# Kernel tuning notes

Measured on AMD Instinct MI355X. Metric: run time of the kernel, lower is better.

Reference implementation:

```python
import jax, jax.numpy as jnp
import numpy as np

B, T, C, H, N = 4, 1024, 1024, 16, 64
DW, DA, DV, DG = 64, 64, 64, 160  # LoRA ranks derived from C=1024
LNX_EPS = 0.00064


def layer_norm(h, g, b, eps=1e-5):
    m = h.mean(-1, keepdims=True)
    var = ((h - m) ** 2).mean(-1, keepdims=True)
    return (h - m) * jax.lax.rsqrt(var + eps) * g + b


def token_shift(h):
    # nn.ZeroPad2d((0,0,1,-1)): shift right along T, zero at t=0
    return jnp.pad(h, ((0, 0), (1, 0), (0, 0)))[:, :-1]


def wkv7(r, w, k, v, a, b):
    # RWKV-7 generalized recurrence. Inputs [B,T,C]; w is log-space decay.
    def re(t):
        return t.reshape(B, T, H, N).transpose(1, 0, 2, 3)  # -> [T,B,H,N]
    r, w, k, v, a, b = map(re, (r, w, k, v, a, b))
    dec = jnp.exp(-jnp.exp(w))
    S0 = jnp.zeros((B, H, N, N), r.dtype)  # state: [value_dim, key_dim]
    def step(S, ins):
        r_, d_, k_, v_, a_, b_ = ins
        sa = jnp.einsum('bhij,bhj->bhi', S, a_)
        S = S * d_[:, :, None, :] + sa[..., None] * b_[:, :, None, :] + v_[..., None] * k_[:, :, None, :]
        return S, jnp.einsum('bhij,bhj->bhi', S, r_)
    _, out = jax.lax.scan(step, S0, (r, dec, k, v, a, b))
    return out.transpose(1, 0, 2, 3).reshape(B, T, C)


def _forward(x, v_first, ln1_g, ln1_b, ln2_g, ln2_b, x_r, x_w, x_k_mix, x_v_mix, x_a, x_g,
             w0, w1, w2, a0, a1, a2, v0, v1, v2, g1, g2, k_k, k_a, r_k,
             W_r, W_k, W_v, W_o, lnx_g, lnx_b, xk_c, Wk_ff, Wv_ff):
    # ---- RNW_Tmix (original RWKV-7 path, layer_id > 0) ----
    h = layer_norm(x, ln1_g, ln1_b)
    xx = token_shift(h) - h
    xr = h + xx * x_r
    xw = h + xx * x_w
    xk = h + xx * x_k_mix
    xv = h + xx * x_v_mix
    xa = h + xx * x_a
    xg = h + xx * x_g
    r = xr @ W_r.T
    w = -jax.nn.softplus(-(w0 + jnp.tanh(xw @ w1) @ w2)) - 0.5
    k = xk @ W_k.T
    v = xv @ W_v.T
    v = v + (v_first - v) * jax.nn.sigmoid(v0 + (xv @ v1) @ v2)
    a = jax.nn.sigmoid(a0 + (xa @ a1) @ a2)
    g = jax.nn.sigmoid(xg @ g1) @ g2
    kk = (k * k_k).reshape(B, T, H, N)
    kk = kk / jnp.maximum(jnp.linalg.norm(kk, axis=-1, keepdims=True), 1e-12)
    kk = kk.reshape(B, T, C)
    k = k * (1 + (a - 1) * k_a)
    y = wkv7(r, w, k, v, -kk, kk * a)
    # GroupNorm(H groups of N channels), eps=0.00064
    yg = y.reshape(B, T, H, N)
    m = yg.mean(-1, keepdims=True)
    var = ((yg - m) ** 2).mean(-1, keepdims=True)
    y = ((yg - m) * jax.lax.rsqrt(var + LNX_EPS)).reshape(B, T, C) * lnx_g + lnx_b
    r4 = r.reshape(B, T, H, N)
    k4 = k.reshape(B, T, H, N)
    v4 = v.reshape(B, T, H, N)
    y = y + ((r4 * k4 * r_k).sum(-1, keepdims=True) * v4).reshape(B, T, C)
    x = x + (y * g) @ W_o.T
    # ---- RWKV_CMix_x070 ----
    h2 = layer_norm(x, ln2_g, ln2_b)
    hx = token_shift(h2) - h2
    kf = h2 + hx * xk_c
    kf = jnp.square(jax.nn.relu(kf @ Wk_ff.T))
    x = x + kf @ Wv_ff.T
    return x


def setup_inputs() -> dict:
    key = jax.random.key(0)
    ks = jax.random.split(key, 40)
    it = iter(range(40))
    def rn(shape, s=0.02):
        return (jax.random.normal(ks[next(it)], shape) * s).astype(jnp.float32)
    def ru(shape):
        return jax.random.uniform(ks[next(it)], shape).astype(jnp.float32)
    return {
        'x': rn((B, T, C), 1.0),
        'v_first': rn((B, T, C), 1.0),
        'ln1_g': jnp.ones((C,), jnp.float32), 'ln1_b': jnp.zeros((C,), jnp.float32),
        'ln2_g': jnp.ones((C,), jnp.float32), 'ln2_b': jnp.zeros((C,), jnp.float32),
        'x_r': ru((1, 1, C)), 'x_w': ru((1, 1, C)), 'x_k_mix': ru((1, 1, C)),
        'x_v_mix': ru((1, 1, C)), 'x_a': ru((1, 1, C)), 'x_g': ru((1, 1, C)),
        'w0': rn((1, 1, C), 0.5) - 4.0, 'w1': rn((C, DW)), 'w2': rn((DW, C), 0.1),
        'a0': rn((1, 1, C), 0.3), 'a1': rn((C, DA)), 'a2': rn((DA, C), 0.1),
        'v0': rn((1, 1, C), 0.3) + 0.73, 'v1': rn((C, DV)), 'v2': rn((DV, C), 0.1),
        'g1': rn((C, DG)), 'g2': rn((DG, C), 0.1),
        'k_k': rn((1, 1, C), 0.05) + 0.71, 'k_a': rn((1, 1, C), 0.05) + 1.02,
        'r_k': rn((H, N), 0.05) - 0.04,
        'W_r': rn((C, C)), 'W_k': rn((C, C), 0.002), 'W_v': rn((C, C)), 'W_o': rn((C, C)),
        'lnx_g': jnp.ones((C,), jnp.float32), 'lnx_b': jnp.zeros((C,), jnp.float32),
        'xk_c': ru((1, 1, C)),
        'Wk_ff': rn((4 * C, C)), 'Wv_ff': rn((C, 4 * C)),
    }


def reference(x, v_first, ln1_g, ln1_b, ln2_g, ln2_b, x_r, x_w, x_k_mix, x_v_mix, x_a, x_g,
              w0, w1, w2, a0, a1, a2, v0, v1, v2, g1, g2, k_k, k_a, r_k,
              W_r, W_k, W_v, W_o, lnx_g, lnx_b, xk_c, Wk_ff, Wv_ff):
    return _forward(x, v_first, ln1_g, ln1_b, ln2_g, ln2_b, x_r, x_w, x_k_mix, x_v_mix, x_a, x_g,
                    w0, w1, w2, a0, a1, a2, v0, v1, v2, g1, g2, k_k, k_a, r_k,
                    W_r, W_k, W_v, W_o, lnx_g, lnx_b, xk_c, Wk_ff, Wv_ff)
```

## Files before the change

kernel.cpp:

```cpp
#include <hip/hip_runtime.h>
#include <hip/hip_bf16.h>


#define BB 4
#define TT 1024
#define CC 1024
#define HH 16
#define NHEAD 64
#define MTOK 4096
#define FFDIM 4096

using bf16 = __hip_bfloat16;
typedef __attribute__((ext_vector_type(8))) short short8;
typedef __attribute__((ext_vector_type(4))) float f32x4;

__device__ __forceinline__ float b2f(bf16 x) { return __bfloat162float(x); }
__device__ __forceinline__ bf16 f2b(float x) { return __float2bfloat16(x); }
__device__ __forceinline__ float u2f(unsigned short u) {
  return __uint_as_float((unsigned)u << 16);
}
__device__ __forceinline__ float4 cv4(ushort4 u) {
  return make_float4(u2f(u.x), u2f(u.y), u2f(u.z), u2f(u.w));
}
__device__ __forceinline__ float ldin(const void* p, size_t i, int m) {
  return m ? b2f(((const bf16*)p)[i]) : ((const float*)p)[i];
}

__device__ __forceinline__ void async16(const void* g, void* l) {
  __builtin_amdgcn_global_load_lds((const __attribute__((address_space(1))) void*)g,
                                   (__attribute__((address_space(3))) void*)l, 16, 0, 0);
}

__device__ __forceinline__ float rowsum16(float x) {
  int t;
  t = __builtin_amdgcn_update_dpp(0, __float_as_int(x), 0x121, 0xF, 0xF, true);
  x += __int_as_float(t);
  t = __builtin_amdgcn_update_dpp(0, __float_as_int(x), 0x122, 0xF, 0xF, true);
  x += __int_as_float(t);
  t = __builtin_amdgcn_update_dpp(0, __float_as_int(x), 0x124, 0xF, 0xF, true);
  x += __int_as_float(t);
  t = __builtin_amdgcn_update_dpp(0, __float_as_int(x), 0x128, 0xF, 0xF, true);
  x += __int_as_float(t);
  return x;
}

__device__ __forceinline__ void rowsum16_2(float& x, float& y) {
  int t1, t2;
  t1 = __builtin_amdgcn_update_dpp(0, __float_as_int(x), 0x121, 0xF, 0xF, true);
  t2 = __builtin_amdgcn_update_dpp(0, __float_as_int(y), 0x121, 0xF, 0xF, true);
  x += __int_as_float(t1); y += __int_as_float(t2);
  t1 = __builtin_amdgcn_update_dpp(0, __float_as_int(x), 0x122, 0xF, 0xF, true);
  t2 = __builtin_amdgcn_update_dpp(0, __float_as_int(y), 0x122, 0xF, 0xF, true);
  x += __int_as_float(t1); y += __int_as_float(t2);
  t1 = __builtin_amdgcn_update_dpp(0, __float_as_int(x), 0x124, 0xF, 0xF, true);
  t2 = __builtin_amdgcn_update_dpp(0, __float_as_int(y), 0x124, 0xF, 0xF, true);
  x += __int_as_float(t1); y += __int_as_float(t2);
  t1 = __builtin_amdgcn_update_dpp(0, __float_as_int(x), 0x128, 0xF, 0xF, true);
  t2 = __builtin_amdgcn_update_dpp(0, __float_as_int(y), 0x128, 0xF, 0xF, true);
  x += __int_as_float(t1); y += __int_as_float(t2);
}

__global__ void probe_kernel(const unsigned int* g, int* flag) {
  if (threadIdx.x == 0 && blockIdx.x == 0) {
    flag[0] = (g[0] == 0x3F800000u) ? 0 : 1;
    flag[1] = 1;
  }
}

__global__ __launch_bounds__(256) void cvt_all(
    const void* wr, const void* wk, const void* wv, const void* wo,
    const void* wkff, const void* wvff, const int* flagp,
    bf16* wrc, bf16* wkc, bf16* wvc, bf16* woc, bf16* wkffc, bf16* wvffc) {
  const int z = blockIdx.z;
  const void* in; bf16* out; int n4;
  const int nCC4 = CC * CC / 4, nFF4 = FFDIM * CC / 4;
  switch (z) {
    case 0: in = wr;   out = wrc;   n4 = nCC4; break;
    case 1: in = wk;   out = wkc;   n4 = nCC4; break;
    case 2: in = wv;   out = wvc;   n4 = nCC4; break;
    case 3: in = wo;   out = woc;   n4 = nCC4; break;
    case 4: in = wkff; out = wkffc; n4 = nFF4; break;
    default: in = wvff; out = wvffc; n4 = nFF4; break;
  }
  const int fl = *flagp;
  const int i4 = blockIdx.x * 256 + threadIdx.x;
  if (i4 >= n4) return;
  const size_t i = (size_t)i4 * 4;
#pragma unroll
  for (int e = 0; e < 4; ++e) out[i + e] = f2b(ldin(in, i + e, fl));
}

__global__ __launch_bounds__(256) void fillmark_kernel(unsigned short* out, int n) {
  const int i = blockIdx.x * 256 + threadIdx.x;
  if (i < n) out[i] = 0x3F80;
}

template<int XM>
__global__ __launch_bounds__(256) void ln_kernel(const void* __restrict__ x,
    const void* __restrict__ g, const void* __restrict__ be, const int* flagp,
    bf16* __restrict__ out, float eps) {
  const int fl = *flagp;
  const int xm = (XM < 0) ? fl : XM;
  const int tid = threadIdx.x;
  const size_t base = (size_t)blockIdx.x * CC + tid * 4;
  float v[4];
#pragma unroll
  for (int e = 0; e < 4; ++e) v[e] = ldin(x, base + e, xm);
  float s  = v[0] + v[1] + v[2] + v[3];
  float ss = v[0]*v[0] + v[1]*v[1] + v[2]*v[2] + v[3]*v[3];
#pragma unroll
  for (int m = 1; m <= 32; m <<= 1) { s += __shfl_xor(s, m); ss += __shfl_xor(ss, m); }
  __shared__ float red[8];
  const int wave = tid >> 6, lane = tid & 63;
  if (lane == 0) { red[wave] = s; red[4 + wave] = ss; }
  __syncthreads();
  s  = red[0] + red[1] + red[2] + red[3];
  ss = red[4] + red[5] + red[6] + red[7];
  const float mean = s * (1.0f / CC);
  const float var  = ss * (1.0f / CC) - mean * mean;
  const float rstd = rsqrtf(var + eps);
#pragma unroll
  for (int e = 0; e < 4; ++e) {
    const int c = tid * 4 + e;
    out[base + e] = f2b((v[e] - mean) * rstd * ldin(g, c, fl) + ldin(be, c, fl));
  }
}

__global__ __launch_bounds__(256) void mix6_kernel(const bf16* __restrict__ h,
    const void* cr, const void* cw, const void* ck,
    const void* cv, const void* ca, const void* cg, const int* flagp,
    bf16* __restrict__ xr, bf16* __restrict__ xw, bf16* __restrict__ xk,
    bf16* __restrict__ xv, bf16* __restrict__ xa, bf16* __restrict__ xg) {
  const int fl = *flagp;
  const size_t idx = (size_t)blockIdx.x * 256 + threadIdx.x;
  const int c = idx & (CC - 1);
  const int t = (idx >> 10) & (TT - 1);
  const float hv = b2f(h[idx]);
  const float xx = (t == 0 ? 0.f : b2f(h[idx - CC])) - hv;
  xr[idx] = f2b(hv + xx * ldin(cr, c, fl));
  xw[idx] = f2b(hv + xx * ldin(cw, c, fl));
  xk[idx] = f2b(hv + xx * ldin(ck, c, fl));
  xv[idx] = f2b(hv + xx * ldin(cv, c, fl));
  xa[idx] = f2b(hv + xx * ldin(ca, c, fl));
  xg[idx] = f2b(hv + xx * ldin(cg, c, fl));
}

__global__ __launch_bounds__(256) void mix1_kernel(const bf16* __restrict__ h,
    const void* cf, const int* flagp, bf16* __restrict__ out) {
  const int fl = *flagp;
  const size_t idx = (size_t)blockIdx.x * 256 + threadIdx.x;
  const int c = idx & (CC - 1);
  const int t = (idx >> 10) & (TT - 1);
  const float hv = b2f(h[idx]);
  const float xx = (t == 0 ? 0.f : b2f(h[idx - CC])) - hv;
  out[idx] = f2b(hv + xx * ldin(cf, c, fl));
}

__global__ __launch_bounds__(256) void transpose_all(
    const void* w1, const void* a1, const void* v1, const void* g1,
    const void* w2, const void* a2, const void* v2, const void* g2,
    const int* flagp,
    bf16* w1t, bf16* a1t, bf16* v1t, bf16* g1t,
    bf16* w2t, bf16* a2t, bf16* v2t, bf16* g2t) {
  const int z = blockIdx.z;
  const void* in; bf16* out; int R, Cc;
  switch (z) {
    case 0: in = w1; out = w1t; R = CC;  Cc = 64;  break;
    case 1: in = a1; out = a1t; R = CC;  Cc = 64;  break;
    case 2: in = v1; out = v1t; R = CC;  Cc = 64;  break;
    case 3: in = g1; out = g1t; R = CC;  Cc = 160; break;
    case 4: in = w2; out = w2t; R = 64;  Cc = CC;  break;
    case 5: in = a2; out = a2t; R = 64;  Cc = CC;  break;
    case 6: in = v2; out = v2t; R = 64;  Cc = CC;  break;
    default: in = g2; out = g2t; R = 160; Cc = CC; break;
  }
  const int fl = *flagp;
  const int idx = blockIdx.x * 256 + threadIdx.x;
  if (idx >= R * Cc) return;
  const int r = idx / Cc, c = idx - r * Cc;
  out[(size_t)c * R + r] = f2b(ldin(in, idx, fl));
}

__device__ __forceinline__ void gemm_core(const bf16* __restrict__ A,
    const bf16* __restrict__ Bm, bf16* __restrict__ Out, int M, int N, int K,
    int mode, short* As, short* Bs) {
  const int tid  = threadIdx.x;
  const int wave = tid >> 6;
  const int lane = tid & 63;
  const int m0 = blockIdx.y * 128;
  const int n0 = blockIdx.x * 128;
  const int wr = (wave >> 1) * 64;
  const int wc = (wave & 1) * 64;
  const int lrow = lane & 15;
  const int lq   = lane >> 4;
  f32x4 acc[4][4];
#pragma unroll
  for (int i = 0; i < 4; ++i)
#pragma unroll
    for (int j = 0; j < 4; ++j) acc[i][j] = (f32x4){0.f, 0.f, 0.f, 0.f};

  for (int k0 = 0; k0 < K; k0 += 32) {
#pragma unroll
    for (int j = 0; j < 2; ++j) {
      const int chunk = j * 256 + tid;
      const int row = chunk >> 2;
      const int c8  = (chunk & 3) * 8;
      const int ldsbase = (j * 256 + wave * 64) * 8;
      const bf16* ga = A + (size_t)(m0 + row) * K + (k0 + c8);
      int br = n0 + row; br = br < N ? br : N - 1;
      const bf16* gb = Bm + (size_t)br * K + (k0 + c8);
      async16(ga, &As[ldsbase]);
      async16(gb, &Bs[ldsbase]);
    }
    __syncthreads();
    short8 af[4], bfr[4];
#pragma unroll
    for (int mi = 0; mi < 4; ++mi)
      af[mi] = *(const short8*)&As[(wr + mi * 16 + lrow) * 32 + lq * 8];
#pragma unroll
    for (int ni = 0; ni < 4; ++ni)
      bfr[ni] = *(const short8*)&Bs[(wc + ni * 16 + lrow) * 32 + lq * 8];
#pragma unroll
    for (int mi = 0; mi < 4; ++mi)
#pragma unroll
      for (int ni = 0; ni < 4; ++ni)
        acc[mi][ni] = __builtin_amdgcn_mfma_f32_16x16x32_bf16(af[mi], bfr[ni], acc[mi][ni], 0, 0, 0);
    __syncthreads();
  }
#pragma unroll
  for (int mi = 0; mi < 4; ++mi) {
#pragma unroll
    for (int ni = 0; ni < 4; ++ni) {
      const int col = n0 + wc + ni * 16 + lrow;
      if (col < N) {
#pragma unroll
        for (int rr = 0; rr < 4; ++rr) {
          const int rowg = m0 + wr + mi * 16 + lq * 4 + rr;
          const size_t oidx = (size_t)rowg * N + col;
          const float val = acc[mi][ni][rr];
          if (mode == 1) { const float t = val > 0.f ? val : 0.f; Out[oidx] = f2b(t * t); }
          else if (mode == 2) Out[oidx] = f2b(val);
          else if (mode == 3) Out[oidx] = f2b(tanhf(val));
          else Out[oidx] = f2b(1.f / (1.f + expf(-val)));
        }
      }
    }
  }
}

template<int MODE>
__global__ __launch_bounds__(256) void gemm_mf(const bf16* __restrict__ A,
    const bf16* __restrict__ Bm, bf16* __restrict__ Out, int M, int N, int K) {
  __shared__ short As[128 * 32];
  __shared__ short Bs[128 * 32];
  gemm_core(A, Bm, Out, M, N, K, MODE, As, Bs);
}

__global__ __launch_bounds__(256) void gemm_lora1(
    const bf16* xw, const bf16* xa, const bf16* xv, const bf16* xg,
    const bf16* w1t, const bf16* a1t, const bf16* v1t, const bf16* g1t,
    bf16* wm, bf16* am, bf16* vm, bf16* gm) {
  __shared__ short As[128 * 32];
  __shared__ short Bs[128 * 32];
  const int z = blockIdx.z;
  const bf16* A; const bf16* B; bf16* O; int N; int mode;
  if (z == 0)      { A = xw; B = w1t; O = wm; N = 64;  mode = 3; }
  else if (z == 1) { A = xa; B = a1t; O = am; N = 64;  mode = 2; }
  else if (z == 2) { A = xv; B = v1t; O = vm; N = 64;  mode = 2; }
  else             { A = xg; B = g1t; O = gm; N = 160; mode = 4; }
  if ((int)blockIdx.x * 128 >= N) return;
  gemm_core(A, B, O, MTOK, N, CC, mode, As, Bs);
}

__global__ __launch_bounds__(256) void gemm_lora2(
    const bf16* wm, const bf16* am, const bf16* vm, const bf16* gm,
    const bf16* w2t, const bf16* a2t, const bf16* v2t, const bf16* g2t,
    bf16* wl, bf16* al, bf16* vl, bf16* gb) {
  __shared__ short As[128 * 32];
  __shared__ short Bs[128 * 32];
  const int z = blockIdx.z;
  const bf16* A; const bf16* B; bf16* O; int K;
  if (z == 0)      { A = wm; B = w2t; O = wl; K = 64;  }
  else if (z == 1) { A = am; B = a2t; O = al; K = 64;  }
  else if (z == 2) { A = vm; B = v2t; O = vl; K = 64;  }
  else             { A = gm; B = g2t; O = gb; K = 160; }
  gemm_core(A, B, O, MTOK, CC, K, 2, As, Bs);
}

template<int MODE>
__global__ __launch_bounds__(256) void gemm_bt(const bf16* __restrict__ A,
    const void* __restrict__ Bm, const int* bmp, bf16* __restrict__ Out,
    int M, int N, int K) {
  const int bm = *bmp;
  __shared__ float As[64][17];
  __shared__ float Bs[64][17];
  const int tid = threadIdx.x;
  const int m0 = blockIdx.y * 64;
  const int n0 = blockIdx.x * 64;
  const int ty = tid >> 4, tx = tid & 15;
  float acc[4][4] = {};
  for (int k0 = 0; k0 < K; k0 += 16) {
    __syncthreads();
#pragma unroll
    for (int e = 0; e < 4; ++e) {
      const int lin = e * 256 + tid;
      const int row = lin >> 4;
      const int kk  = lin & 15;
      As[row][kk] = b2f(A[(size_t)(m0 + row) * K + k0 + kk]);
      int br = n0 + row; br = br < N ? br : N - 1;
      Bs[row][kk] = ldin(Bm, (size_t)br * K + k0 + kk, bm);
    }
    __syncthreads();
#pragma unroll
    for (int k = 0; k < 16; ++k) {
      float a[4], b[4];
#pragma unroll
      for (int i = 0; i < 4; ++i) a[i] = As[ty * 4 + i][k];
#pragma unroll
      for (int j = 0; j < 4; ++j) b[j] = Bs[tx * 4 + j][k];
#pragma unroll
      for (int i = 0; i < 4; ++i)
#pragma unroll
        for (int j = 0; j < 4; ++j) acc[i][j] += a[i] * b[j];
    }
  }
#pragma unroll
  for (int i = 0; i < 4; ++i) {
    const int rowg = m0 + ty * 4 + i;
#pragma unroll
    for (int j = 0; j < 4; ++j) {
      const int col = n0 + tx * 4 + j;
      if (col < N) {
        const size_t oidx = (size_t)rowg * N + col;
        const float val = acc[i][j];
        if (MODE == 1) { const float t = val > 0.f ? val : 0.f; Out[oidx] = f2b(t * t); }
        else if (MODE == 2) Out[oidx] = f2b(val);
        else if (MODE == 3) Out[oidx] = f2b(tanhf(val));
        else Out[oidx] = f2b(1.f / (1.f + expf(-val)));
      }
    }
  }
}

__global__ __launch_bounds__(256) void combine_kernel(
    bf16* kf, bf16* vf, bf16* wl, bf16* al, bf16* vl,
    const void* vfirst, const void* w0, const void* a0, const void* v0,
    const void* kkp, const void* kap, const int* flagp, float* decp) {
  const int fl = *flagp;
  const int tid = threadIdx.x;
  const size_t base = (size_t)blockIdx.x * CC + tid * 4;
  float kkv[4], av4[4];
  float ssq = 0.f;
#pragma unroll
  for (int e = 0; e < 4; ++e) {
    const int c = tid * 4 + e;
    const size_t idx = base + e;
    const float u = ldin(w0, c, fl) + b2f(wl[idx]);
    const float w = (u > 0.f ? -log1pf(expf(-u)) : u - log1pf(expf(u))) - 0.5f;
    wl[idx] = f2b(w);
    if (decp) decp[idx] = __expf(-__expf(w));
    const float a  = 1.f / (1.f + expf(-(ldin(a0, c, fl) + b2f(al[idx]))));
    const float vg = 1.f / (1.f + expf(-(ldin(v0, c, fl) + b2f(vl[idx]))));
    const float v = b2f(vf[idx]);
    vf[idx] = f2b(v + (ldin(vfirst, idx, fl) - v) * vg);
    const float kv = b2f(kf[idx]);
    const float kkr = kv * ldin(kkp, c, fl);
    kkv[e] = kkr; av4[e] = a;
    ssq += kkr * kkr;
    kf[idx] = f2b(kv * (1.f + (a - 1.f) * ldin(kap, c, fl)));
  }
  ssq += __shfl_xor(ssq, 1); ssq += __shfl_xor(ssq, 2);
  ssq += __shfl_xor(ssq, 4); ssq += __shfl_xor(ssq, 8);
  const float inv = 1.f / fmaxf(sqrtf(ssq), 1e-12f);
#pragma unroll
  for (int e = 0; e < 4; ++e) {
    const size_t idx = base + e;
    const float kkn = kkv[e] * inv;
    al[idx] = f2b(-kkn);
    vl[idx] = f2b(kkn * av4[e]);
  }
}


template<int DF>
__device__ __forceinline__ void wkv_stage(const bf16* rp, const void* wp,
    const bf16* kp, const bf16* vp, const bf16* ap, const bf16* bp,
    size_t cb, char* sb, int wave, int lane) {
  const int hb = wave & 1;
  const size_t g2 = cb + (size_t)(hb * 8 + (lane >> 3)) * CC + (lane & 7) * 8;
  if (wave < 2) {
    async16(rp + g2, sb + 0    + hb * 1024);
    async16(kp + g2, sb + 2048 + hb * 1024);
    async16(ap + g2, sb + 4096 + hb * 1024);
  } else {
    async16(bp + g2, sb + 6144 + hb * 1024);
    async16(vp + g2, sb + 8192 + hb * 1024);
  }
  if constexpr (DF) {
    const size_t gd = cb + (size_t)(wave * 4 + (lane >> 4)) * CC + (lane & 15) * 4;
    async16((const float*)wp + gd, sb + 10240 + wave * 1024);
  } else {
    if (wave >= 2) async16((const bf16*)wp + g2, sb + 10240 + hb * 1024);
  }
}

template<int DF>
__device__ __forceinline__ void wkv_load_step(const char* sb, int t, int j0, int i,
    float4& rv, float4& dv, float4& av, float4& bv, float4& vk) {
  const short* sR = (const short*)sb;
  const short* sK = (const short*)(sb + 2048);
  const short* sA = (const short*)(sb + 4096);
  const short* sB = (const short*)(sb + 6144);
  const unsigned short* sV = (const unsigned short*)(sb + 8192);
  rv = cv4(*(const ushort4*)(const void*)(sR + t * 64 + j0));
  const float4 kv = cv4(*(const ushort4*)(const void*)(sK + t * 64 + j0));
  av = cv4(*(const ushort4*)(const void*)(sA + t * 64 + j0));
  bv = cv4(*(const ushort4*)(const void*)(sB + t * 64 + j0));
  const float vi = u2f(sV[t * 64 + i]);
  if constexpr (DF) {
    const float* sD = (const float*)(sb + 10240);
    dv = *(const float4*)(const void*)(sD + t * 64 + j0);
  } else {
    const short* sW = (const short*)(sb + 10240);
    const float4 wv = cv4(*(const ushort4*)(const void*)(sW + t * 64 + j0));
    dv = make_float4(__expf(-__expf(wv.x)), __expf(-__expf(wv.y)),
                     __expf(-__expf(wv.z)), __expf(-__expf(wv.w)));
  }
  vk = make_float4(vi * kv.x, vi * kv.y, vi * kv.z, vi * kv.w);
}

template<int DF>
__global__ __launch_bounds__(256) void wkv_scan(
    const bf16* __restrict__ rp, const void* __restrict__ wp,
    const bf16* __restrict__ kp, const bf16* __restrict__ vp,
    const bf16* __restrict__ ap, const bf16* __restrict__ bp,
    bf16* __restrict__ yp) {
  constexpr int BUFB = DF ? 14336 : 12288;
  __shared__ char sbuf[2][BUFB];
  const int blk = blockIdx.x;
  const int q = blk & 3;
  const int h = (blk >> 2) & (HH - 1);
  const int b = blk >> 6;
  const int tid = threadIdx.x;
  const int wave = tid >> 6;
  const int lane = tid & 63;
  const int rl = tid >> 4;
  const int jq = tid & 15;
  const int j0 = jq * 4;
  const int i = q * 16 + rl;
  const size_t bbase = (size_t)b * TT * CC + (size_t)h * NHEAD;

  float4 S = make_float4(0.f, 0.f, 0.f, 0.f);

  wkv_stage<DF>(rp, wp, kp, vp, ap, bp, bbase, sbuf[0], wave, lane);
  __syncthreads();

  for (int c = 0; c < TT / 16; ++c) {
    if (c + 1 < TT / 16)
      wkv_stage<DF>(rp, wp, kp, vp, ap, bp, bbase + (size_t)(c + 1) * 16 * CC,
                    sbuf[(c + 1) & 1], wave, lane);
    const char* sb = sbuf[c & 1];

    float4 rv, dv, av, bv, vk;
    wkv_load_step<DF>(sb, 0, j0, i, rv, dv, av, bv, vk);
    float qv_prev = 0.f;
    float ocol = 0.f;
#pragma unroll
    for (int s = 0; s < 16; ++s) {
      float4 rv2, dv2, av2, bv2, vk2;
      if (s + 1 < 16)
        wkv_load_step<DF>(sb, s + 1, j0, i, rv2, dv2, av2, bv2, vk2);
      float p = (S.x * av.x + S.y * av.y) + (S.z * av.z + S.w * av.w);
      if (s == 0) {
        p = rowsum16(p);
      } else {
        rowsum16_2(p, qv_prev);
        ocol = (jq == s - 1) ? qv_prev : ocol;
      }
      const float sa = p;
      S.x = fmaf(S.x, dv.x, fmaf(sa, bv.x, vk.x));
      S.y = fmaf(S.y, dv.y, fmaf(sa, bv.y, vk.y));
      S.z = fmaf(S.z, dv.z, fmaf(sa, bv.z, vk.z));
      S.w = fmaf(S.w, dv.w, fmaf(sa, bv.w, vk.w));
      qv_prev = (S.x * rv.x + S.y * rv.y) + (S.z * rv.z + S.w * rv.w);
      if (s + 1 < 16) { rv = rv2; dv = dv2; av = av2; bv = bv2; vk = vk2; }
    }
    qv_prev = rowsum16(qv_prev);
    ocol = (jq == 15) ? qv_prev : ocol;
    yp[bbase + (size_t)(c * 16 + jq) * CC + i] = f2b(ocol);
    __syncthreads();
  }
}

__global__ __launch_bounds__(256) void post_kernel(
    const bf16* __restrict__ y, const bf16* __restrict__ rp, const bf16* __restrict__ kp,
    const bf16* __restrict__ vp, const bf16* __restrict__ gp,
    const void* rk, const void* lnxg, const void* lnxb, const int* flagp,
    bf16* __restrict__ out) {
  const int fl = *flagp;
  const int tid = threadIdx.x;
  const size_t base = (size_t)blockIdx.x * CC + tid * 4;
  float yv[4];
  float s = 0.f, ssq = 0.f, dot = 0.f;
#pragma unroll
  for (int e = 0; e < 4; ++e) {
    const size_t idx = base + e;
    yv[e] = b2f(y[idx]);
    s += yv[e]; ssq += yv[e] * yv[e];
    dot += b2f(rp[idx]) * b2f(kp[idx]) * ldin(rk, tid * 4 + e, fl);
  }
  s   += __shfl_xor(s, 1);   s   += __shfl_xor(s, 2);   s   += __shfl_xor(s, 4);   s   += __shfl_xor(s, 8);
  ssq += __shfl_xor(ssq, 1); ssq += __shfl_xor(ssq, 2); ssq += __shfl_xor(ssq, 4); ssq += __shfl_xor(ssq, 8);
  dot += __shfl_xor(dot, 1); dot += __shfl_xor(dot, 2); dot += __shfl_xor(dot, 4); dot += __shfl_xor(dot, 8);
  const float m = s * (1.f / NHEAD);
  const float var = ssq * (1.f / NHEAD) - m * m;
  const float rs = rsqrtf(var + 0.00064f);
#pragma unroll
  for (int e = 0; e < 4; ++e) {
    const int c = tid * 4 + e;
    const size_t idx = base + e;
    const float yo = (yv[e] - m) * rs * ldin(lnxg, c, fl) + ldin(lnxb, c, fl)
                     + dot * b2f(vp[idx]);
    out[idx] = f2b(yo * b2f(gp[idx]));
  }
}

__global__ __launch_bounds__(256) void addres_kernel(const void* x, const int* flagp,
    const bf16* __restrict__ o, float* __restrict__ out) {
  const int fl = *flagp;
  const size_t idx = (size_t)blockIdx.x * 256 + threadIdx.x;
  out[idx] = ldin(x, idx, fl) + b2f(o[idx]);
}

__global__ __launch_bounds__(256) void final_kernel(const float* __restrict__ x1,
    const bf16* __restrict__ f, const int* flagp, void* out) {
  const int fl = *flagp;
  const size_t idx = (size_t)blockIdx.x * 256 + threadIdx.x;
  const float v = x1[idx] + b2f(f[idx]);
  if (fl) ((bf16*)out)[idx] = f2b(v);
  else    ((float*)out)[idx] = v;
}

extern "C" void kernel_launch(void* const* d_in, const int* in_sizes, int n_in,
                              void* d_out, int out_size, void* d_ws, size_t ws_size,
                              hipStream_t stream) {
  const void* X      = d_in[0];
  const void* VFIRST = d_in[1];
  const void* LN1G = d_in[2];
  const void* LN1B = d_in[3];
  const void* LN2G = d_in[4];
  const void* LN2B = d_in[5];
  const void* XRC = d_in[6];
  const void* XWC = d_in[7];
  const void* XKC = d_in[8];
  const void* XVC = d_in[9];
  const void* XAC = d_in[10];
  const void* XGC = d_in[11];
  const void* W0p = d_in[12];
  const void* W1p = d_in[13];
  const void* W2p = d_in[14];
  const void* A0p = d_in[15];
  const void* A1p = d_in[16];
  const void* A2p = d_in[17];
  const void* V0p = d_in[18];
  const void* V1p = d_in[19];
  const void* V2p = d_in[20];
  const void* G1p = d_in[21];
  const void* G2p = d_in[22];
  const void* KKp = d_in[23];
  const void* KAp = d_in[24];
  const void* RKp = d_in[25];
  const void* WR  = d_in[26];
  const void* WK  = d_in[27];
  const void* WV  = d_in[28];
  const void* WO  = d_in[29];
  const void* LNXG = d_in[30];
  const void* LNXB = d_in[31];
  const void* XKCF = d_in[32];
  const void* WKFF = d_in[33];
  const void* WVFF = d_in[34];

  const size_t BTC  = (size_t)MTOK * CC;
  const size_t SLOT = BTC * 2;
  char* ws = (char*)d_ws;

  size_t off = 8 * SLOT;
  auto alloc = [&](size_t n) { size_t o = off; off += (n + 255) & ~(size_t)255; return o; };
  const size_t oW1T = alloc((size_t)CC * 64 * 2);
  const size_t oA1T = alloc((size_t)CC * 64 * 2);
  const size_t oV1T = alloc((size_t)CC * 64 * 2);
  const size_t oG1T = alloc((size_t)CC * 160 * 2);
  const size_t oW2T = alloc((size_t)CC * 64 * 2);
  const size_t oA2T = alloc((size_t)CC * 64 * 2);
  const size_t oV2T = alloc((size_t)CC * 64 * 2);
  const size_t oG2T = alloc((size_t)CC * 160 * 2);
  const size_t oWM  = alloc((size_t)MTOK * 64 * 2);
  const size_t oAM  = alloc((size_t)MTOK * 64 * 2);
  const size_t oVM  = alloc((size_t)MTOK * 64 * 2);
  const size_t oGM  = alloc((size_t)MTOK * 160 * 2);
  const size_t oFLG = alloc(8);
  const size_t baseNeed = off;
  const size_t oDEC = alloc(BTC * 4);
  const size_t decNeed = off;
  const size_t oWRc   = alloc((size_t)CC * CC * 2);
  const size_t oWKc   = alloc((size_t)CC * CC * 2);
  const size_t oWVc   = alloc((size_t)CC * CC * 2);
  const size_t oWOc   = alloc((size_t)CC * CC * 2);
  const size_t oWKFFc = alloc((size_t)FFDIM * CC * 2);
  const size_t oWVFFc = alloc((size_t)CC * FFDIM * 2);
  const size_t mfmaNeed = off;

  if (baseNeed > ws_size) {
    fillmark_kernel<<<(out_size + 255) / 256, 256, 0, stream>>>(
        (unsigned short*)d_out, out_size);
    return;
  }
  const bool hasdec = (decNeed <= ws_size);
  const bool useMF  = (mfmaNeed <= ws_size);

  int* FLAG = (int*)(ws + oFLG);
  int* ONE  = FLAG + 1;

  bf16* B0 = (bf16*)(ws + 0 * SLOT);
  bf16* B1 = (bf16*)(ws + 1 * SLOT);
  bf16* B2 = (bf16*)(ws + 2 * SLOT);
  bf16* B3 = (bf16*)(ws + 3 * SLOT);
  bf16* B4 = (bf16*)(ws + 4 * SLOT);
  bf16* B5 = (bf16*)(ws + 5 * SLOT);
  bf16* B6 = (bf16*)(ws + 6 * SLOT);
  bf16* B7 = (bf16*)(ws + 7 * SLOT);
  bf16* Hb  = B0;
  bf16* XRb = B1; bf16* XWb = B2; bf16* XKb = B3;
  bf16* XVb = B4; bf16* XAb = B5; bf16* XGb = B6;
  bf16* Rb  = B7;
  bf16* Kg  = B0;
  bf16* Vg  = B1;
  bf16* WLb = B2;
  bf16* ALb = B3;
  bf16* VLb = B4;
  bf16* Gb  = B5;
  bf16* Yb  = B6;
  bf16* YG  = B2;
  bf16* OBb = B0;
  float* X1b = (float*)(ws + 2 * SLOT);
  bf16* H2b  = B1;
  bf16* KFIN = B0;
  bf16* KACT = B4;
  bf16* FFNb = B1;

  bf16* W1T = (bf16*)(ws + oW1T);
  bf16* A1T = (bf16*)(ws + oA1T);
  bf16* V1T = (bf16*)(ws + oV1T);
  bf16* G1T = (bf16*)(ws + oG1T);
  bf16* W2T = (bf16*)(ws + oW2T);
  bf16* A2T = (bf16*)(ws + oA2T);
  bf16* V2T = (bf16*)(ws + oV2T);
  bf16* G2T = (bf16*)(ws + oG2T);
  bf16* WM  = (bf16*)(ws + oWM);
  bf16* AM  = (bf16*)(ws + oAM);
  bf16* VM  = (bf16*)(ws + oVM);
  bf16* GM  = (bf16*)(ws + oGM);
  float* DECb = (float*)(ws + oDEC);
  float* DECarg = hasdec ? DECb : (float*)nullptr;
  bf16* WRc   = (bf16*)(ws + oWRc);
  bf16* WKc   = (bf16*)(ws + oWKc);
  bf16* WVc   = (bf16*)(ws + oWVc);
  bf16* WOc   = (bf16*)(ws + oWOc);
  bf16* WKFFc = (bf16*)(ws + oWKFFc);
  bf16* WVFFc = (bf16*)(ws + oWVFFc);

  const int EW = (int)(BTC / 256);
  const dim3 blk256(256);

  probe_kernel<<<1, 1, 0, stream>>>((const unsigned int*)LN1G, FLAG);

  ln_kernel<-1><<<MTOK, blk256, 0, stream>>>(X, LN1G, LN1B, FLAG, Hb, 1e-5f);
  mix6_kernel<<<EW, blk256, 0, stream>>>(Hb, XRC, XWC, XKC, XVC, XAC, XGC, FLAG,
                                         XRb, XWb, XKb, XVb, XAb, XGb);
  transpose_all<<<dim3(640, 1, 8), blk256, 0, stream>>>(
      W1p, A1p, V1p, G1p, W2p, A2p, V2p, G2p, FLAG,
      W1T, A1T, V1T, G1T, W2T, A2T, V2T, G2T);

  if (useMF) {
    cvt_all<<<dim3(4096, 1, 6), blk256, 0, stream>>>(
        WR, WK, WV, WO, WKFF, WVFF, FLAG, WRc, WKc, WVc, WOc, WKFFc, WVFFc);

    const dim3 gCC(8, 32), gFF1(32, 32);
    gemm_lora1<<<dim3(2, 32, 4), blk256, 0, stream>>>(
        XWb, XAb, XVb, XGb, W1T, A1T, V1T, G1T, WM, AM, VM, GM);
    gemm_mf<2><<<gCC, blk256, 0, stream>>>(XRb, WRc, Rb, MTOK, CC, CC);
    gemm_mf<2><<<gCC, blk256, 0, stream>>>(XKb, WKc, Kg, MTOK, CC, CC);
    gemm_mf<2><<<gCC, blk256, 0, stream>>>(XVb, WVc, Vg, MTOK, CC, CC);
    gemm_lora2<<<dim3(8, 32, 4), blk256, 0, stream>>>(
        WM, AM, VM, GM, W2T, A2T, V2T, G2T, WLb, ALb, VLb, Gb);

    combine_kernel<<<MTOK, blk256, 0, stream>>>(Kg, Vg, WLb, ALb, VLb, VFIRST,
                                                W0p, A0p, V0p, KKp, KAp, FLAG, DECarg);
    if (hasdec)
      wkv_scan<1><<<BB * HH * 4, blk256, 0, stream>>>(Rb, DECb, Kg, Vg, ALb, VLb, Yb);
    else
      wkv_scan<0><<<BB * HH * 4, blk256, 0, stream>>>(Rb, WLb, Kg, Vg, ALb, VLb, Yb);
    post_kernel<<<MTOK, blk256, 0, stream>>>(Yb, Rb, Kg, Vg, Gb, RKp, LNXG, LNXB, FLAG, YG);
    gemm_mf<2><<<gCC, blk256, 0, stream>>>(YG, WOc, OBb, MTOK, CC, CC);
    addres_kernel<<<EW, blk256, 0, stream>>>(X, FLAG, OBb, X1b);

    ln_kernel<0><<<MTOK, blk256, 0, stream>>>(X1b, LN2G, LN2B, FLAG, H2b, 1e-5f);
    mix1_kernel<<<EW, blk256, 0, stream>>>(H2b, XKCF, FLAG, KFIN);
    gemm_mf<1><<<gFF1, blk256, 0, stream>>>(KFIN, WKFFc, KACT, MTOK, FFDIM, CC);
    gemm_mf<2><<<gCC, blk256, 0, stream>>>(KACT, WVFFc, FFNb, MTOK, CC, FFDIM);
    final_kernel<<<EW, blk256, 0, stream>>>(X1b, FFNb, FLAG, d_out);
  } else {
    const dim3 gCC(16, 64), gL1(1, 64), gG1(3, 64), gFF1(64, 64);
    gemm_bt<3><<<gL1, blk256, 0, stream>>>(XWb, W1T, ONE, WM, MTOK, 64, CC);
    gemm_bt<2><<<gL1, blk256, 0, stream>>>(XAb, A1T, ONE, AM, MTOK, 64, CC);
    gemm_bt<2><<<gL1, blk256, 0, stream>>>(XVb, V1T, ONE, VM, MTOK, 64, CC);
    gemm_bt<4><<<gG1, blk256, 0, stream>>>(XGb, G1T, ONE, GM, MTOK, 160, CC);
    gemm_bt<2><<<gCC, blk256, 0, stream>>>(XRb, WR, FLAG, Rb, MTOK, CC, CC);
    gemm_bt<2><<<gCC, blk256, 0, stream>>>(XKb, WK, FLAG, Kg, MTOK, CC, CC);
    gemm_bt<2><<<gCC, blk256, 0, stream>>>(XVb, WV, FLAG, Vg, MTOK, CC, CC);
    gemm_bt<2><<<gCC, blk256, 0, stream>>>(WM, W2T, ONE, WLb, MTOK, CC, 64);
    gemm_bt<2><<<gCC, blk256, 0, stream>>>(AM, A2T, ONE, ALb, MTOK, CC, 64);
    gemm_bt<2><<<gCC, blk256, 0, stream>>>(VM, V2T, ONE, VLb, MTOK, CC, 64);
    gemm_bt<2><<<gCC, blk256, 0, stream>>>(GM, G2T, ONE, Gb, MTOK, CC, 160);

    combine_kernel<<<MTOK, blk256, 0, stream>>>(Kg, Vg, WLb, ALb, VLb, VFIRST,
                                                W0p, A0p, V0p, KKp, KAp, FLAG, DECarg);
    if (hasdec)
      wkv_scan<1><<<BB * HH * 4, blk256, 0, stream>>>(Rb, DECb, Kg, Vg, ALb, VLb, Yb);
    else
      wkv_scan<0><<<BB * HH * 4, blk256, 0, stream>>>(Rb, WLb, Kg, Vg, ALb, VLb, Yb);
    post_kernel<<<MTOK, blk256, 0, stream>>>(Yb, Rb, Kg, Vg, Gb, RKp, LNXG, LNXB, FLAG, YG);
    gemm_bt<2><<<gCC, blk256, 0, stream>>>(YG, WO, FLAG, OBb, MTOK, CC, CC);
    addres_kernel<<<EW, blk256, 0, stream>>>(X, FLAG, OBb, X1b);

    ln_kernel<0><<<MTOK, blk256, 0, stream>>>(X1b, LN2G, LN2B, FLAG, H2b, 1e-5f);
    mix1_kernel<<<EW, blk256, 0, stream>>>(H2b, XKCF, FLAG, KFIN);
    gemm_bt<1><<<gFF1, blk256, 0, stream>>>(KFIN, WKFF, FLAG, KACT, MTOK, FFDIM, CC);
    gemm_bt<2><<<gCC, blk256, 0, stream>>>(KACT, WVFF, FLAG, FFNb, MTOK, CC, FFDIM);
    final_kernel<<<EW, blk256, 0, stream>>>(X1b, FFNb, FLAG, d_out);
  }

  (void)in_sizes; (void)n_in; (void)out_size;
}
```

Before: 796.4 us.

## Batch R/K projections with LoRA GEMMs, split-K FFN down-proj, fuse residual+LN

Merges the R and K projection GEMMs into the LoRA-down launch as extra z-slices so more blocks run concurrently in one launch. The FFN down-projection (K=4096) is split into two K halves written as fp32 partials, then summed with the residual in a new final kernel. The residual add and the second LayerNorm are fused into one kernel. The goal is higher occupancy and fewer launches and memory passes, at the cost of extra fp32 partial traffic and additional workspace.

```diff
diff --git a/kernel.cpp b/kernel.cpp
--- a/kernel.cpp
+++ b/kernel.cpp
@@ -123,6 +123,39 @@
   for (int e = 0; e < 4; ++e) {
     const int c = tid * 4 + e;
     out[base + e] = f2b((v[e] - mean) * rstd * ldin(g, c, fl) + ldin(be, c, fl));
+  }
+}
+
+__global__ __launch_bounds__(256) void addln_kernel(const void* __restrict__ x,
+    const bf16* __restrict__ ob, const void* __restrict__ g,
+    const void* __restrict__ be, const int* flagp,
+    float* __restrict__ x1, bf16* __restrict__ h2, float eps) {
+  const int fl = *flagp;
+  const int tid = threadIdx.x;
+  const size_t base = (size_t)blockIdx.x * CC + tid * 4;
+  float v[4];
+#pragma unroll
+  for (int e = 0; e < 4; ++e) {
+    v[e] = ldin(x, base + e, fl) + b2f(ob[base + e]);
+    x1[base + e] = v[e];
+  }
+  float s  = v[0] + v[1] + v[2] + v[3];
+  float ss = v[0]*v[0] + v[1]*v[1] + v[2]*v[2] + v[3]*v[3];
+#pragma unroll
+  for (int m = 1; m <= 32; m <<= 1) { s += __shfl_xor(s, m); ss += __shfl_xor(ss, m); }
+  __shared__ float red[8];
+  const int wave = tid >> 6, lane = tid & 63;
+  if (lane == 0) { red[wave] = s; red[4 + wave] = ss; }
+  __syncthreads();
+  s  = red[0] + red[1] + red[2] + red[3];
+  ss = red[4] + red[5] + red[6] + red[7];
+  const float mean = s * (1.0f / CC);
+  const float var  = ss * (1.0f / CC) - mean * mean;
+  const float rstd = rsqrtf(var + eps);
+#pragma unroll
+  for (int e = 0; e < 4; ++e) {
+    const int c = tid * 4 + e;
+    h2[base + e] = f2b((v[e] - mean) * rstd * ldin(g, c, fl) + ldin(be, c, fl));
   }
 }
 
@@ -183,7 +216,7 @@
 
 __device__ __forceinline__ void gemm_core(const bf16* __restrict__ A,
     const bf16* __restrict__ Bm, bf16* __restrict__ Out, int M, int N, int K,
-    int mode, short* As, short* Bs) {
+    int lda, int ldb, int mode, short* As, short* Bs) {
   const int tid  = threadIdx.x;
   const int wave = tid >> 6;
   const int lane = tid & 63;
@@ -206,9 +239,9 @@
       const int row = chunk >> 2;
       const int c8  = (chunk & 3) * 8;
       const int ldsbase = (j * 256 + wave * 64) * 8;
-      const bf16* ga = A + (size_t)(m0 + row) * K + (k0 + c8);
+      const bf16* ga = A + (size_t)(m0 + row) * lda + (k0 + c8);
       int br = n0 + row; br = br < N ? br : N - 1;
-      const bf16* gb = Bm + (size_t)br * K + (k0 + c8);
+      const bf16* gb = Bm + (size_t)br * ldb + (k0 + c8);
       async16(ga, &As[ldsbase]);
       async16(gb, &Bs[ldsbase]);
     }
@@ -241,7 +274,8 @@
           if (mode == 1) { const float t = val > 0.f ? val : 0.f; Out[oidx] = f2b(t * t); }
           else if (mode == 2) Out[oidx] = f2b(val);
           else if (mode == 3) Out[oidx] = f2b(tanhf(val));
-          else Out[oidx] = f2b(1.f / (1.f + expf(-val)));
+          else if (mode == 4) Out[oidx] = f2b(1.f / (1.f + expf(-val)));
+          else ((float*)Out)[oidx] = val;
         }
       }
     }
@@ -253,23 +287,28 @@
     const bf16* __restrict__ Bm, bf16* __restrict__ Out, int M, int N, int K) {
   __shared__ short As[128 * 32];
   __shared__ short Bs[128 * 32];
-  gemm_core(A, Bm, Out, M, N, K, MODE, As, Bs);
-}
-
-__global__ __launch_bounds__(256) void gemm_lora1(
+  gemm_core(A, Bm, Out, M, N, K, K, K, MODE, As, Bs);
+}
+
+__global__ __launch_bounds__(256) void gemm_qkl(
     const bf16* xw, const bf16* xa, const bf16* xv, const bf16* xg,
+    const bf16* xr, const bf16* xk,
     const bf16* w1t, const bf16* a1t, const bf16* v1t, const bf16* g1t,
-    bf16* wm, bf16* am, bf16* vm, bf16* gm) {
+    const bf16* wrc, const bf16* wkc,
+    bf16* wm, bf16* am, bf16* vm, bf16* gm,
+    bf16* rb, bf16* kg) {
   __shared__ short As[128 * 32];
   __shared__ short Bs[128 * 32];
   const int z = blockIdx.z;
   const bf16* A; const bf16* B; bf16* O; int N; int mode;
-  if (z == 0)      { A = xw; B = w1t; O = wm; N = 64;  mode = 3; }
-  else if (z == 1) { A = xa; B = a1t; O = am; N = 64;  mode = 2; }
-  else if (z == 2) { A = xv; B = v1t; O = vm; N = 64;  mode = 2; }
-  else             { A = xg; B = g1t; O = gm; N = 160; mode = 4; }
+  if (z == 0)      { A = xw;  B = w1t; O = wm; N = 64;  mode = 3; }
+  else if (z == 1) { A = xa;  B = a1t; O = am; N = 64;  mode = 2; }
+  else if (z == 2) { A = xv;  B = v1t; O = vm; N = 64;  mode = 2; }
+  else if (z == 3) { A = xg;  B = g1t; O = gm; N = 160; mode = 4; }
+  else if (z == 4) { A = xr;  B = wrc; O = rb; N = CC;  mode = 2; }
+  else             { A = xk;  B = wkc; O = kg; N = CC;  mode = 2; }
   if ((int)blockIdx.x * 128 >= N) return;
-  gemm_core(A, B, O, MTOK, N, CC, mode, As, Bs);
+  gemm_core(A, B, O, MTOK, N, CC, CC, CC, mode, As, Bs);
 }
 
 __global__ __launch_bounds__(256) void gemm_lora2(
@@ -284,7 +323,19 @@
   else if (z == 1) { A = am; B = a2t; O = al; K = 64;  }
   else if (z == 2) { A = vm; B = v2t; O = vl; K = 64;  }
   else             { A = gm; B = g2t; O = gb; K = 160; }
-  gemm_core(A, B, O, MTOK, CC, K, 2, As, Bs);
+  gemm_core(A, B, O, MTOK, CC, K, K, K, 2, As, Bs);
+}
+
+__global__ __launch_bounds__(256) void gemm_ff2sk(
+    const bf16* __restrict__ kact, const bf16* __restrict__ wvffc,
+    float* p0, float* p1) {
+  __shared__ short As[128 * 32];
+  __shared__ short Bs[128 * 32];
+  const int z = blockIdx.z;
+  const int koff = z * (FFDIM / 2);
+  float* P = z ? p1 : p0;
+  gemm_core(kact + koff, wvffc + koff, (bf16*)P, MTOK, CC, FFDIM / 2,
+            FFDIM, FFDIM, 5, As, Bs);
 }
 
 template<int MODE>
@@ -537,6 +588,16 @@
   const int fl = *flagp;
   const size_t idx = (size_t)blockIdx.x * 256 + threadIdx.x;
   const float v = x1[idx] + b2f(f[idx]);
+  if (fl) ((bf16*)out)[idx] = f2b(v);
+  else    ((float*)out)[idx] = v;
+}
+
+__global__ __launch_bounds__(256) void final_sk_kernel(const float* __restrict__ x1,
+    const float* __restrict__ p0, const float* __restrict__ p1,
+    const int* flagp, void* out) {
+  const int fl = *flagp;
+  const size_t idx = (size_t)blockIdx.x * 256 + threadIdx.x;
+  const float v = x1[idx] + (p0[idx] + p1[idx]);
   if (fl) ((bf16*)out)[idx] = f2b(v);
   else    ((float*)out)[idx] = v;
 }
@@ -609,6 +670,9 @@
   const size_t oWKFFc = alloc((size_t)FFDIM * CC * 2);
   const size_t oWVFFc = alloc((size_t)CC * FFDIM * 2);
   const size_t mfmaNeed = off;
+  const size_t oP0 = alloc(BTC * 4);
+  const size_t oP1 = alloc(BTC * 4);
+  const size_t ff2Need = off;
 
   if (baseNeed > ws_size) {
     fillmark_kernel<<<(out_size + 255) / 256, 256, 0, stream>>>(
@@ -617,6 +681,7 @@
   }
   const bool hasdec = (decNeed <= ws_size);
   const bool useMF  = (mfmaNeed <= ws_size);
+  const bool hasff2 = (ff2Need <= ws_size);
 
   int* FLAG = (int*)(ws + oFLG);
   int* ONE  = FLAG + 1;
@@ -668,6 +733,8 @@
   bf16* WOc   = (bf16*)(ws + oWOc);
   bf16* WKFFc = (bf16*)(ws + oWKFFc);
   bf16* WVFFc = (bf16*)(ws + oWVFFc);
+  float* P0 = (float*)(ws + oP0);
+  float* P1 = (float*)(ws + oP1);
 
   const int EW = (int)(BTC / 256);
   const dim3 blk256(256);
@@ -686,10 +753,10 @@
         WR, WK, WV, WO, WKFF, WVFF, FLAG, WRc, WKc, WVc, WOc, WKFFc, WVFFc);
 
     const dim3 gCC(8, 32), gFF1(32, 32);
-    gemm_lora1<<<dim3(2, 32, 4), blk256, 0, stream>>>(
-        XWb, XAb, XVb, XGb, W1T, A1T, V1T, G1T, WM, AM, VM, GM);
-    gemm_mf<2><<<gCC, blk256, 0, stream>>>(XRb, WRc, Rb, MTOK, CC, CC);
-    gemm_mf<2><<<gCC, blk256, 0, stream>>>(XKb, WKc, Kg, MTOK, CC, CC);
+    gemm_qkl<<<dim3(8, 32, 6), blk256, 0, stream>>>(
+        XWb, XAb, XVb, XGb, XRb, XKb,
+        W1T, A1T, V1T, G1T, WRc, WKc,
+        WM, AM, VM, GM, Rb, Kg);
     gemm_mf<2><<<gCC, blk256, 0, stream>>>(XVb, WVc, Vg, MTOK, CC, CC);
     gemm_lora2<<<dim3(8, 32, 4), blk256, 0, stream>>>(
         WM, AM, VM, GM, W2T, A2T, V2T, G2T, WLb, ALb, VLb, Gb);
@@ -702,13 +769,17 @@
       wkv_scan<0><<<BB * HH * 4, blk256, 0, stream>>>(Rb, WLb, Kg, Vg, ALb, VLb, Yb);
     post_kernel<<<MTOK, blk256, 0, stream>>>(Yb, Rb, Kg, Vg, Gb, RKp, LNXG, LNXB, FLAG, YG);
     gemm_mf<2><<<gCC, blk256, 0, stream>>>(YG, WOc, OBb, MTOK, CC, CC);
-    addres_kernel<<<EW, blk256, 0, stream>>>(X, FLAG, OBb, X1b);
-
-    ln_kernel<0><<<MTOK, blk256, 0, stream>>>(X1b, LN2G, LN2B, FLAG, H2b, 1e-5f);
+    addln_kernel<<<MTOK, blk256, 0, stream>>>(X, OBb, LN2G, LN2B, FLAG, X1b, H2b, 1e-5f);
+
     mix1_kernel<<<EW, blk256, 0, stream>>>(H2b, XKCF, FLAG, KFIN);
     gemm_mf<1><<<gFF1, blk256, 0, stream>>>(KFIN, WKFFc, KACT, MTOK, FFDIM, CC);
-    gemm_mf<2><<<gCC, blk256, 0, stream>>>(KACT, WVFFc, FFNb, MTOK, CC, FFDIM);
-    final_kernel<<<EW, blk256, 0, stream>>>(X1b, FFNb, FLAG, d_out);
+    if (hasff2) {
+      gemm_ff2sk<<<dim3(8, 32, 2), blk256, 0, stream>>>(KACT, WVFFc, P0, P1);
+      final_sk_kernel<<<EW, blk256, 0, stream>>>(X1b, P0, P1, FLAG, d_out);
+    } else {
+      gemm_mf<2><<<gCC, blk256, 0, stream>>>(KACT, WVFFc, FFNb, MTOK, CC, FFDIM);
+      final_kernel<<<EW, blk256, 0, stream>>>(X1b, FFNb, FLAG, d_out);
+    }
   } else {
     const dim3 gCC(16, 64), gL1(1, 64), gG1(3, 64), gFF1(64, 64);
     gemm_bt<3><<<gL1, blk256, 0, stream>>>(XWb, W1T, ONE, WM, MTOK, 64, CC);
@@ -731,9 +802,8 @@
       wkv_scan<0><<<BB * HH * 4, blk256, 0, stream>>>(Rb, WLb, Kg, Vg, ALb, VLb, Yb);
     post_kernel<<<MTOK, blk256, 0, stream>>>(Yb, Rb, Kg, Vg, Gb, RKp, LNXG, LNXB, FLAG, YG);
     gemm_bt<2><<<gCC, blk256, 0, stream>>>(YG, WO, FLAG, OBb, MTOK, CC, CC);
-    addres_kernel<<<EW, blk256, 0, stream>>>(X, FLAG, OBb, X1b);
-
-    ln_kernel<0><<<MTOK, blk256, 0, stream>>>(X1b, LN2G, LN2B, FLAG, H2b, 1e-5f);
+    addln_kernel<<<MTOK, blk256, 0, stream>>>(X, OBb, LN2G, LN2B, FLAG, X1b, H2b, 1e-5f);
+
     mix1_kernel<<<EW, blk256, 0, stream>>>(H2b, XKCF, FLAG, KFIN);
     gemm_bt<1><<<gFF1, blk256, 0, stream>>>(KFIN, WKFF, FLAG, KACT, MTOK, FFDIM, CC);
     gemm_bt<2><<<gCC, blk256, 0, stream>>>(KACT, WVFF, FLAG, FFNb, MTOK, CC, FFDIM);
```

Result: faster. 779.9 us (-2.1%).
